# Kernel tuning notes

Hardware: AMD Instinct MI355X
Metric: run time of the kernel (lower is better)

The kernel has to match this reference:

```python
import jax, jax.numpy as jnp
import numpy as np

EPS = 1e-7
TAU = 2.0  # curr_temp = max_temp at init
GROUPS = 2
NUM_CODES = 320


def setup_inputs() -> dict:
    key = jax.random.key(0)
    k1, k2, k3, k4 = jax.random.split(key, 4)
    B, T, C = 8, 2048, 1024
    GV = GROUPS * NUM_CODES  # 640
    D = 256
    x = jax.random.normal(k1, (B, T, C), dtype=jnp.float32)
    W = jax.random.normal(k2, (GV, C), dtype=jnp.float32)  # nn.init.normal_(std=1)
    b = jnp.zeros((GV,), dtype=jnp.float32)
    codebook = jax.random.uniform(k3, (1, GV, D), dtype=jnp.float32)  # uniform_ init
    u = jax.random.uniform(k4, (B * T * GROUPS, NUM_CODES), dtype=jnp.float32,
                           minval=1e-10, maxval=1.0)
    gumbel_noise = -jnp.log(-jnp.log(u))
    return {"x": x, "W": W, "b": b, "codebook": codebook, "gumbel_noise": gumbel_noise}


def reference(x, W, b, codebook, gumbel_noise):
    B, T, C = x.shape
    N = B * T
    G, V = GROUPS, NUM_CODES
    D = codebook.shape[-1]

    # weight projection -> logits [N, G*V]
    logits = jnp.einsum('nc,vc->nv', x.reshape(N, C), W) + b
    l = logits.reshape(N * G, V)

    # hard codes (no-grad path in torch)
    k = jnp.argmax(l, axis=-1)
    hard_x = jax.nn.one_hot(k, V, dtype=l.dtype).reshape(N, G, V)
    hard_probs = jax.lax.stop_gradient(hard_x).mean(axis=0)  # [G, V]
    code_perplexity = jnp.exp(-jnp.sum(hard_probs * jnp.log(hard_probs + EPS), axis=-1)).sum()

    avg_probs = jax.nn.softmax(l.reshape(N, G, V), axis=-1).mean(axis=0)  # [G, V]
    prob_perplexity = jnp.exp(-jnp.sum(avg_probs * jnp.log(avg_probs + EPS), axis=-1)).sum()

    # gumbel-softmax, hard=True with straight-through (training path)
    y_soft = jax.nn.softmax((l + gumbel_noise) / TAU, axis=-1)  # [N*G, V]
    idx = jnp.argmax(y_soft, axis=-1)
    y_hard = jax.nn.one_hot(idx, V, dtype=y_soft.dtype)
    y = y_hard + y_soft - jax.lax.stop_gradient(y_soft)

    # combine with codebook: (onehot-ish weights) @ codebook per group
    q = jnp.einsum('ngv,gvd->ngd', y.reshape(N, G, V), codebook.reshape(G, V, D))
    q = q.reshape(B, T, G * D)

    num_vars = G * V
    diversity_loss = (num_vars - prob_perplexity) / num_vars
    return q, code_perplexity, prob_perplexity, diversity_loss
```

## Files before the change

kernel.cpp:

```cpp
#include <hip/hip_runtime.h>

#define N_ROWS 16384
#define C_DIM  1024
#define GV     640
#define V_DIM  320
#define G_DIM  2
#define D_DIM  256
#define MROWS  64
#define FBLKS  (N_ROWS / MROWS)
#define NBUCKET 64

typedef __attribute__((ext_vector_type(8))) _Float16 half8;
typedef __attribute__((ext_vector_type(4))) _Float16 half4v;
typedef __attribute__((ext_vector_type(4))) float float4v;

#define LDS_AS(p) ((__attribute__((address_space(3))) unsigned int*)(p))
#define GLB_AS(p) ((const __attribute__((address_space(1))) unsigned int*)(p))

__global__ __launch_bounds__(256) void wsplit_kernel(const float* __restrict__ src,
                                                     _Float16* __restrict__ dst,
                                                     int* __restrict__ zr) {
  const int t = blockIdx.x * 256 + threadIdx.x;
  zr[t] = 0;
  const int n = t % GV;
  const int cc = t / GV;
  const int k = cc * 8;
  const float4 v0 = *(const float4*)(src + (size_t)n * C_DIM + k);
  const float4 v1 = *(const float4*)(src + (size_t)n * C_DIM + k + 4);
  half8 h;
  h[0] = (_Float16)v0.x; h[1] = (_Float16)v0.y; h[2] = (_Float16)v0.z; h[3] = (_Float16)v0.w;
  h[4] = (_Float16)v1.x; h[5] = (_Float16)v1.y; h[6] = (_Float16)v1.z; h[7] = (_Float16)v1.w;
  *(half8*)(dst + (size_t)t * 8) = h;
}

__global__ __launch_bounds__(512, 2) void fused_kernel(
    const float* __restrict__ x,
    const _Float16* __restrict__ whT,
    const float* __restrict__ bias,
    const float* __restrict__ gn,
    const float* __restrict__ cb,
    float* __restrict__ q,
    float* __restrict__ mf,
    int* __restrict__ mi) {
  __shared__ __align__(16) char smemU[98304];
  _Float16* BhL = (_Float16*)smemU;
  _Float16* AhL = (_Float16*)(smemU + 81920);
  _Float16* AlL = (_Float16*)(smemU + 90112);
  float* Ldump  = (float*)smemU;
  __shared__ float accL[GV];
  __shared__ int   cntL[GV];

  const int tid = threadIdx.x;
  const int lane = tid & 63;
  const int w = tid >> 6;
  const int m0 = blockIdx.x * MROWS;
  const int frow = lane & 15;
  const int quad = lane >> 4;

  for (int e = tid; e < GV; e += 512) { accL[e] = 0.0f; cntL[e] = 0; }

  const int ar = tid >> 3;
  const int ak = (tid & 7) * 4;
  const int ac = ak >> 3;
  const int ah_off = ak & 7;
  const float* xp = x + (size_t)(m0 + ar) * C_DIM + ak;

  float4v acc[4][5];
#pragma unroll
  for (int i = 0; i < 4; ++i)
#pragma unroll
    for (int j = 0; j < 5; ++j) acc[i][j] = (float4v)0.0f;

  auto stageB = [&](int kb, _Float16* Bh) {
    const _Float16* bsrc = whT + (size_t)kb * 2560 * 8;
#pragma unroll
    for (int s = 0; s < 5; ++s) {
      const int c = s * 512 + tid;
      __builtin_amdgcn_global_load_lds(GLB_AS(bsrc + (size_t)c * 8),
                                       LDS_AS(Bh + c * 8), 16, 0, 0);
    }
  };
  auto splitA = [&](const float4& a4, _Float16* Ah, _Float16* Al) {
    const _Float16 h0 = (_Float16)a4.x, h1 = (_Float16)a4.y;
    const _Float16 h2 = (_Float16)a4.z, h3 = (_Float16)a4.w;
    half4v hv, lv;
    hv[0] = h0; hv[1] = h1; hv[2] = h2; hv[3] = h3;
    lv[0] = (_Float16)(a4.x - (float)h0);
    lv[1] = (_Float16)(a4.y - (float)h1);
    lv[2] = (_Float16)(a4.z - (float)h2);
    lv[3] = (_Float16)(a4.w - (float)h3);
    *(half4v*)&Ah[(ac * 64 + ar) * 8 + ah_off] = hv;
    *(half4v*)&Al[(ac * 64 + ar) * 8 + ah_off] = lv;
  };

  float4 a4 = *(const float4*)xp;
  stageB(0, BhL);
  splitA(a4, AhL, AlL);
  a4 = *(const float4*)(xp + 32);
  __syncthreads();

  for (int kb = 0; kb < 32; ++kb) {
    const int cur = kb & 1;
    _Float16* BhC = BhL + cur * 20480;
    _Float16* AhC = AhL + cur * 2048;
    _Float16* AlC = AlL + cur * 2048;

    if (kb < 31) {
      const int nxt = cur ^ 1;
      stageB(kb + 1, BhL + nxt * 20480);
      splitA(a4, AhL + nxt * 2048, AlL + nxt * 2048);
      if (kb < 30) a4 = *(const float4*)(xp + (kb + 2) * 32);
    }

    half8 ah[4], al[4];
#pragma unroll
    for (int i = 0; i < 4; ++i) {
      ah[i] = *(const half8*)&AhC[(quad * 64 + 16 * i + frow) * 8];
      al[i] = *(const half8*)&AlC[(quad * 64 + 16 * i + frow) * 8];
    }
#pragma unroll
    for (int j = 0; j < 5; ++j) {
      const half8 bh = *(const half8*)&BhC[(quad * 640 + 80 * w + 16 * j + frow) * 8];
#pragma unroll
      for (int i = 0; i < 4; ++i) {
        acc[i][j] = __builtin_amdgcn_mfma_f32_16x16x32_f16(ah[i], bh, acc[i][j], 0, 0, 0);
        acc[i][j] = __builtin_amdgcn_mfma_f32_16x16x32_f16(al[i], bh, acc[i][j], 0, 0, 0);
      }
    }
    __syncthreads();
  }

  float bw[5];
#pragma unroll
  for (int j = 0; j < 5; ++j) bw[j] = bias[80 * w + 16 * j + frow];

  const int rl = tid >> 4;
  const int h  = tid & 15;

#pragma unroll
  for (int g = 0; g < G_DIM; ++g) {
#pragma unroll
    for (int hh = 0; hh < 2; ++hh) {
      __syncthreads();
      if ((w >> 2) == g) {
        const int cg0 = 80 * (w & 3) + frow;
#pragma unroll
        for (int ii = 0; ii < 2; ++ii) {
          const int i = 2 * hh + ii;
#pragma unroll
          for (int j = 0; j < 5; ++j)
#pragma unroll
            for (int r = 0; r < 4; ++r)
              Ldump[(16 * ii + 4 * quad + r) * 324 + cg0 + 16 * j] = acc[i][j][r] + bw[j];
        }
      }
      __syncthreads();

      const int n = m0 + hh * 32 + rl;
      const float* gp = gn + (size_t)(2 * n + g) * V_DIM + 20 * h;
      const float* lp = Ldump + rl * 324 + 20 * h;

      float4v L[5], T[5];
      float m = -3.0e38f, tm = -3.0e38f;
      int midx = 0, tidx = 0;
#pragma unroll
      for (int cc = 0; cc < 5; ++cc) {
        const float4v lv = *(const float4v*)(lp + 4 * cc);
        const float4v gv = *(const float4v*)(gp + 4 * cc);
        float4v tv;
#pragma unroll
        for (int e2 = 0; e2 < 4; ++e2) tv[e2] = (lv[e2] + gv[e2]) * 0.5f;
        L[cc] = lv; T[cc] = tv;
#pragma unroll
        for (int e2 = 0; e2 < 4; ++e2) {
          const int v = 20 * h + 4 * cc + e2;
          if (lv[e2] > m)  { m = lv[e2];  midx = v; }
          if (tv[e2] > tm) { tm = tv[e2]; tidx = v; }
        }
      }
#pragma unroll
      for (int off = 8; off > 0; off >>= 1) {
        const float om = __shfl_xor(m, off, 64);
        const int   oi = __shfl_xor(midx, off, 64);
        if (om > m || (om == m && oi < midx)) { m = om; midx = oi; }
        const float ot  = __shfl_xor(tm, off, 64);
        const int   oti = __shfl_xor(tidx, off, 64);
        if (ot > tm || (ot == tm && oti < tidx)) { tm = ot; tidx = oti; }
      }

      float sl = 0.0f, st = 0.0f;
#pragma unroll
      for (int cc = 0; cc < 5; ++cc)
#pragma unroll
        for (int e2 = 0; e2 < 4; ++e2) {
          const float el = expf(L[cc][e2] - m);
          L[cc][e2] = el;
          sl += el;
          st += expf(T[cc][e2] - tm);
        }
#pragma unroll
      for (int off = 8; off > 0; off >>= 1) {
        sl += __shfl_xor(sl, off, 64);
        st += __shfl_xor(st, off, 64);
      }
      const float inv = 1.0f / sl;
      const float sv = 1.0f / st;
      const float yv = (1.0f + sv) - sv;

#pragma unroll
      for (int cc = 0; cc < 5; ++cc)
#pragma unroll
        for (int e2 = 0; e2 < 4; ++e2)
          atomicAdd(&accL[g * V_DIM + 20 * h + 4 * cc + e2], L[cc][e2] * inv);
      if (h == 0) atomicAdd(&cntL[g * V_DIM + midx], 1);

      const float4v* cbp = (const float4v*)cb + (size_t)(g * V_DIM + tidx) * 64;
      float4v* qp = (float4v*)q + (size_t)n * 128 + g * 64;
#pragma unroll
      for (int k2 = 0; k2 < 4; ++k2) {
        const float4v c4 = cbp[h + 16 * k2];
        float4v o4;
#pragma unroll
        for (int e2 = 0; e2 < 4; ++e2) o4[e2] = yv * c4[e2];
        qp[h + 16 * k2] = o4;
      }
    }
  }

  __syncthreads();
  const size_t pb = (size_t)(blockIdx.x & (NBUCKET - 1)) * GV;
  for (int e = tid; e < GV; e += 512) {
    atomicAdd(&mf[pb + e], accL[e]);
    atomicAdd(&mi[pb + e], cntL[e]);
  }
}

__global__ __launch_bounds__(640) void finalize_kernel(
    const float* __restrict__ mf, const int* __restrict__ mi,
    float* __restrict__ out3) {
  __shared__ float sA[G_DIM];
  __shared__ float sC[G_DIM];
  const int t = threadIdx.x;
  if (t < G_DIM) { sA[t] = 0.0f; sC[t] = 0.0f; }
  __syncthreads();

  const int g = t / V_DIM;
  float f = 0.0f;
  int   c = 0;
#pragma unroll 8
  for (int b = 0; b < NBUCKET; ++b) {
    f += mf[(size_t)b * GV + t];
    c += mi[(size_t)b * GV + t];
  }
  const float pa = f * (1.0f / 16384.0f);
  const float ph = (float)c * (1.0f / 16384.0f);
  float a = pa * logf(pa + 1e-7f);
  float h = ph * logf(ph + 1e-7f);
#pragma unroll
  for (int off = 32; off > 0; off >>= 1) {
    a += __shfl_xor(a, off, 64);
    h += __shfl_xor(h, off, 64);
  }
  if ((t & 63) == 0) {
    atomicAdd(&sA[g], a);
    atomicAdd(&sC[g], h);
  }
  __syncthreads();
  if (t == 0) {
    const float code_p = expf(-sC[0]) + expf(-sC[1]);
    const float prob_p = expf(-sA[0]) + expf(-sA[1]);
    out3[0] = code_p;
    out3[1] = prob_p;
    out3[2] = ((float)GV - prob_p) / (float)GV;
  }
}

extern "C" void kernel_launch(void* const* d_in, const int* in_sizes, int n_in,
                              void* d_out, int out_size, void* d_ws, size_t ws_size,
                              hipStream_t stream) {
  const float* x  = (const float*)d_in[0];
  const float* W  = (const float*)d_in[1];
  const float* b  = (const float*)d_in[2];
  const float* cb = (const float*)d_in[3];
  const float* gn = (const float*)d_in[4];
  float* out = (float*)d_out;

  char* ws = (char*)d_ws;
  _Float16* whT = (_Float16*)ws;
  float* mf = (float*)(ws + 1310720);
  int*   mi = (int*)  (ws + 1474560);

  wsplit_kernel<<<(GV * C_DIM / 8) / 256, 256, 0, stream>>>(W, whT, (int*)mf);

  fused_kernel<<<FBLKS, 512, 0, stream>>>(x, whT, b, gn, cb, out, mf, mi);

  finalize_kernel<<<1, 640, 0, stream>>>(mf, mi, out + (size_t)N_ROWS * 512);
}
```

Baseline: 233.9 us.

## Compute softmax/argmax epilogue directly from MFMA registers instead of LDS dump

The epilogue no longer dumps logits to LDS in four passes. Each wave now computes partial max, argmax and exp-sums straight from its MFMA accumulator fragments, combines them across 16 lanes with shuffles, and merges the four per-wave partials through a small LDS table. Soft-probability column sums are accumulated per lane in registers before one atomic per column, which cuts LDS atomics from one per element to a few per thread. This removes several barriers and a large amount of LDS traffic, but the gumbel-noise reads become strided per lane (16 consecutive floats per access group), and it adds an extra exp rescale and a serial 128-thread merge phase.

```diff
diff --git a/kernel.cpp b/kernel.cpp
--- a/kernel.cpp
+++ b/kernel.cpp
@@ -46,7 +46,8 @@
   _Float16* BhL = (_Float16*)smemU;
   _Float16* AhL = (_Float16*)(smemU + 81920);
   _Float16* AlL = (_Float16*)(smemU + 90112);
-  float* Ldump  = (float*)smemU;
+  float* combW  = (float*)smemU;
+  float* wbL    = (float*)(smemU + 18432);
   __shared__ float accL[GV];
   __shared__ int   cntL[GV];
 
@@ -134,97 +135,128 @@
 #pragma unroll
   for (int j = 0; j < 5; ++j) bw[j] = bias[80 * w + 16 * j + frow];
 
-  const int rl = tid >> 4;
-  const int h  = tid & 15;
-
-#pragma unroll
-  for (int g = 0; g < G_DIM; ++g) {
-#pragma unroll
-    for (int hh = 0; hh < 2; ++hh) {
-      __syncthreads();
-      if ((w >> 2) == g) {
-        const int cg0 = 80 * (w & 3) + frow;
-#pragma unroll
-        for (int ii = 0; ii < 2; ++ii) {
-          const int i = 2 * hh + ii;
-#pragma unroll
-          for (int j = 0; j < 5; ++j)
-#pragma unroll
-            for (int r = 0; r < 4; ++r)
-              Ldump[(16 * ii + 4 * quad + r) * 324 + cg0 + 16 * j] = acc[i][j][r] + bw[j];
-        }
-      }
-      __syncthreads();
-
-      const int n = m0 + hh * 32 + rl;
-      const float* gp = gn + (size_t)(2 * n + g) * V_DIM + 20 * h;
-      const float* lp = Ldump + rl * 324 + 20 * h;
-
-      float4v L[5], T[5];
-      float m = -3.0e38f, tm = -3.0e38f;
-      int midx = 0, tidx = 0;
-#pragma unroll
-      for (int cc = 0; cc < 5; ++cc) {
-        const float4v lv = *(const float4v*)(lp + 4 * cc);
-        const float4v gv = *(const float4v*)(gp + 4 * cc);
-        float4v tv;
-#pragma unroll
-        for (int e2 = 0; e2 < 4; ++e2) tv[e2] = (lv[e2] + gv[e2]) * 0.5f;
-        L[cc] = lv; T[cc] = tv;
-#pragma unroll
-        for (int e2 = 0; e2 < 4; ++e2) {
-          const int v = 20 * h + 4 * cc + e2;
-          if (lv[e2] > m)  { m = lv[e2];  midx = v; }
-          if (tv[e2] > tm) { tm = tv[e2]; tidx = v; }
-        }
-      }
-#pragma unroll
-      for (int off = 8; off > 0; off >>= 1) {
-        const float om = __shfl_xor(m, off, 64);
-        const int   oi = __shfl_xor(midx, off, 64);
-        if (om > m || (om == m && oi < midx)) { m = om; midx = oi; }
-        const float ot  = __shfl_xor(tm, off, 64);
-        const int   oti = __shfl_xor(tidx, off, 64);
-        if (ot > tm || (ot == tm && oti < tidx)) { tm = ot; tidx = oti; }
-      }
-
+  const int g  = w >> 2;
+  const int wq = w & 3;
+
+  float mlk[4][4];
+#pragma unroll
+  for (int i = 0; i < 4; ++i) {
+#pragma unroll
+    for (int r = 0; r < 4; ++r) {
+      const int row = 16 * i + 4 * quad + r;
+      const int n = m0 + row;
+      const float* gp = gn + (size_t)(2 * n + g) * V_DIM + 80 * wq + frow;
+
+      float l5[5], t5[5];
+#pragma unroll
+      for (int j = 0; j < 5; ++j) {
+        l5[j] = acc[i][j][r] + bw[j];
+        t5[j] = (l5[j] + gp[16 * j]) * 0.5f;
+      }
+      float ml = l5[0]; int il = 80 * wq + frow;
+      float mt = t5[0]; int it = il;
+#pragma unroll
+      for (int j = 1; j < 5; ++j) {
+        const int cj = 80 * wq + 16 * j + frow;
+        if (l5[j] > ml) { ml = l5[j]; il = cj; }
+        if (t5[j] > mt) { mt = t5[j]; it = cj; }
+      }
+#pragma unroll
+      for (int off = 1; off < 16; off <<= 1) {
+        const float o1 = __shfl_xor(ml, off, 64); const int i1 = __shfl_xor(il, off, 64);
+        if (o1 > ml || (o1 == ml && i1 < il)) { ml = o1; il = i1; }
+        const float o2 = __shfl_xor(mt, off, 64); const int i2 = __shfl_xor(it, off, 64);
+        if (o2 > mt || (o2 == mt && i2 < it)) { mt = o2; it = i2; }
+      }
+      mlk[i][r] = ml;
       float sl = 0.0f, st = 0.0f;
 #pragma unroll
-      for (int cc = 0; cc < 5; ++cc)
-#pragma unroll
-        for (int e2 = 0; e2 < 4; ++e2) {
-          const float el = expf(L[cc][e2] - m);
-          L[cc][e2] = el;
-          sl += el;
-          st += expf(T[cc][e2] - tm);
-        }
-#pragma unroll
-      for (int off = 8; off > 0; off >>= 1) {
+      for (int j = 0; j < 5; ++j) {
+        const float el = expf(l5[j] - ml);
+        acc[i][j][r] = el;
+        sl += el;
+        st += expf(t5[j] - mt);
+      }
+#pragma unroll
+      for (int off = 1; off < 16; off <<= 1) {
         sl += __shfl_xor(sl, off, 64);
         st += __shfl_xor(st, off, 64);
       }
-      const float inv = 1.0f / sl;
-      const float sv = 1.0f / st;
-      const float yv = (1.0f + sv) - sv;
-
-#pragma unroll
-      for (int cc = 0; cc < 5; ++cc)
-#pragma unroll
-        for (int e2 = 0; e2 < 4; ++e2)
-          atomicAdd(&accL[g * V_DIM + 20 * h + 4 * cc + e2], L[cc][e2] * inv);
-      if (h == 0) atomicAdd(&cntL[g * V_DIM + midx], 1);
-
-      const float4v* cbp = (const float4v*)cb + (size_t)(g * V_DIM + tidx) * 64;
-      float4v* qp = (float4v*)q + (size_t)n * 128 + g * 64;
-#pragma unroll
-      for (int k2 = 0; k2 < 4; ++k2) {
-        const float4v c4 = cbp[h + 16 * k2];
-        float4v o4;
-#pragma unroll
-        for (int e2 = 0; e2 < 4; ++e2) o4[e2] = yv * c4[e2];
-        qp[h + 16 * k2] = o4;
-      }
-    }
+      if (frow == 4 * i + r) {
+        float* dst = combW + (size_t)(g * 64 + row) * 36 + wq * 8;
+        float4v p1, p2;
+        p1[0] = ml; p1[1] = __int_as_float(il); p1[2] = sl; p1[3] = 0.0f;
+        p2[0] = mt; p2[1] = __int_as_float(it); p2[2] = st; p2[3] = 0.0f;
+        *(float4v*)dst = p1;
+        *(float4v*)(dst + 4) = p2;
+      }
+    }
+  }
+  __syncthreads();
+
+  if (tid < 128) {
+    const int rg = tid;
+    const float* cw = combW + (size_t)rg * 36;
+    float mw[4], sw[4], tw[4], s2[4];
+    int   iw[4], ti4[4];
+#pragma unroll
+    for (int v = 0; v < 4; ++v) {
+      const float4v p1 = *(const float4v*)(cw + v * 8);
+      const float4v p2 = *(const float4v*)(cw + v * 8 + 4);
+      mw[v] = p1[0]; iw[v] = __float_as_int(p1[1]); sw[v] = p1[2];
+      tw[v] = p2[0]; ti4[v] = __float_as_int(p2[1]); s2[v] = p2[2];
+    }
+    float m = mw[0]; int idx = iw[0];
+    float tm = tw[0]; int ti = ti4[0];
+#pragma unroll
+    for (int v = 1; v < 4; ++v) {
+      if (mw[v] > m || (mw[v] == m && iw[v] < idx)) { m = mw[v]; idx = iw[v]; }
+      if (tw[v] > tm || (tw[v] == tm && ti4[v] < ti)) { tm = tw[v]; ti = ti4[v]; }
+    }
+    float sl = 0.0f, st = 0.0f;
+#pragma unroll
+    for (int v = 0; v < 4; ++v) {
+      sl += sw[v] * expf(mw[v] - m);
+      st += s2[v] * expf(tw[v] - tm);
+    }
+    const float inv = 1.0f / sl;
+    const float sv = 1.0f / st;
+    const float yv = (1.0f + sv) - sv;
+    const int g2 = rg >> 6;
+    atomicAdd(&cntL[g2 * V_DIM + idx], 1);
+    float4v wbv;
+    wbv[0] = m; wbv[1] = inv; wbv[2] = yv; wbv[3] = __int_as_float(ti);
+    *(float4v*)(wbL + (size_t)rg * 4) = wbv;
+  }
+  __syncthreads();
+
+  float p5[5] = {0.0f, 0.0f, 0.0f, 0.0f, 0.0f};
+#pragma unroll
+  for (int i = 0; i < 4; ++i)
+#pragma unroll
+    for (int r = 0; r < 4; ++r) {
+      const int row = 16 * i + 4 * quad + r;
+      const float4v wbv = *(const float4v*)(wbL + (size_t)(g * 64 + row) * 4);
+      const float k = expf(mlk[i][r] - wbv[0]) * wbv[1];
+#pragma unroll
+      for (int j = 0; j < 5; ++j) p5[j] += acc[i][j][r] * k;
+    }
+#pragma unroll
+  for (int j = 0; j < 5; ++j)
+    atomicAdd(&accL[g * V_DIM + 80 * wq + 16 * j + frow], p5[j]);
+
+#pragma unroll
+  for (int it2 = 0; it2 < 16; ++it2) {
+    const int task = w + 8 * it2;
+    const int tg = task >> 6, trow = task & 63;
+    const float4v wbv = *(const float4v*)(wbL + (size_t)task * 4);
+    const float yv = wbv[2];
+    const int ti = __float_as_int(wbv[3]);
+    const float4v c4 = ((const float4v*)cb)[(size_t)(tg * V_DIM + ti) * 64 + lane];
+    float4v o4;
+#pragma unroll
+    for (int e2 = 0; e2 < 4; ++e2) o4[e2] = yv * c4[e2];
+    ((float4v*)q)[(size_t)(m0 + trow) * 128 + tg * 64 + lane] = o4;
   }
 
   __syncthreads();
```

Measured after the change: 203.1 us. -13.2%, faster.
